# Performance work log

Hardware: AMD Instinct MI355X
Metric: run time of the kernel (lower is better)

## Reference

```python
import jax, jax.numpy as jnp
import numpy as np

H = 16            # num heads (sharded)
NOPE = 128        # qk_nope_head_dim
ROPE = 64         # qk_rope_head_dim
VD = 128          # v_head_dim
KV_RANK = 512
HEAD = NOPE + ROPE  # 192
SCALE = HEAD ** (-0.5)  # mscale == 1 (no yarn scaling)
EPS = 1e-6


def rmsnorm(x, w):
    var = jnp.mean(x * x, axis=-1, keepdims=True)
    return x * jax.lax.rsqrt(var + EPS) * w


def apply_rope(pe, cos, sin):
    # pe: [T, h, ROPE]; torch code de-interleaves pairs then applies
    # non-interleaved (rotate-half) rope: out = [e*cos - o*sin, o*cos + e*sin]
    e = pe[..., 0::2]
    o = pe[..., 1::2]
    c = cos[:, None, :]
    s = sin[:, None, :]
    return jnp.concatenate([e * c - o * s, o * c + e * s], axis=-1)


def setup_inputs() -> dict:
    key = jax.random.key(0)
    ks = jax.random.split(key, 10)
    T, D = 4096, 2048
    w = 0.02
    return {
        "hidden_states": jax.random.normal(ks[0], (T, D), jnp.float32),
        "cos": jax.random.uniform(ks[1], (T, ROPE // 2), jnp.float32),
        "sin": jax.random.uniform(ks[2], (T, ROPE // 2), jnp.float32),
        "w_q_a": jax.random.normal(ks[3], (D, 1536), jnp.float32) * w,
        "q_a_ln_w": jnp.ones((1536,), jnp.float32),
        "w_q_b": jax.random.normal(ks[4], (1536, H * HEAD), jnp.float32) * w,
        "w_kv_a": jax.random.normal(ks[5], (D, KV_RANK + ROPE), jnp.float32) * w,
        "kv_a_ln_w": jnp.ones((KV_RANK,), jnp.float32),
        "w_kv_b": jax.random.normal(ks[6], (KV_RANK, H * (NOPE + VD)), jnp.float32) * w,
        "w_o": jax.random.normal(ks[7], (H * VD, D), jnp.float32) * w,
        "batch_size": 2,
    }


def reference(hidden_states, cos, sin, w_q_a, q_a_ln_w, w_q_b, w_kv_a,
              kv_a_ln_w, w_kv_b, w_o, batch_size):
    T, D = hidden_states.shape
    B = int(batch_size)
    S = T // B

    # Q: low-rank down proj -> RMSNorm -> up proj
    q = rmsnorm(hidden_states @ w_q_a, q_a_ln_w) @ w_q_b
    q = q.reshape(T, H, HEAD)
    q_nope = q[..., :NOPE]
    q_pe = apply_rope(q[..., NOPE:], cos, sin)

    # KV: joint down proj with shared rope part (MQA-style)
    ckv = hidden_states @ w_kv_a                        # [T, 512+64]
    compressed_kv = ckv[:, :KV_RANK]
    k_pe = apply_rope(ckv[:, KV_RANK:][:, None, :], cos, sin)  # [T, 1, 64]
    kv = (rmsnorm(compressed_kv, kv_a_ln_w) @ w_kv_b).reshape(T, H, NOPE + VD)
    k_nope = kv[..., :NOPE]
    v = kv[..., NOPE:]                                   # [T, H, 128]

    # Assemble full query/key heads (value pad to 192 + final slice is a no-op
    # mathematically since padded dims are zero; we keep value dim = 128).
    query = jnp.concatenate([q_nope, q_pe], axis=-1)     # [T, H, 192]
    key = jnp.concatenate([k_nope, jnp.broadcast_to(k_pe, (T, H, ROPE))], axis=-1)

    # Causal (prefill) attention per sequence
    qb = query.reshape(B, S, H, HEAD)
    kb = key.reshape(B, S, H, HEAD)
    vb = v.reshape(B, S, H, VD)
    scores = jnp.einsum("bqhd,bkhd->bhqk", qb, kb) * SCALE
    causal = jnp.tril(jnp.ones((S, S), bool))
    scores = jnp.where(causal, scores, jnp.finfo(scores.dtype).min)
    probs = jax.nn.softmax(scores, axis=-1)
    attn = jnp.einsum("bhqk,bkhd->bqhd", probs, vb)      # [B, S, H, 128]

    return attn.reshape(T, H * VD) @ w_o
```

## Files before the change

kernel.cpp:

```cpp
#include <hip/hip_runtime.h>
#include <cstdint>
#include <cstddef>

#define TT 4096
#define DD 2048
#define NH 16
#define HEADD 192
#define NOPE 128
#define VDIM 128
#define SEQ 2048

typedef __bf16 bf16x8 __attribute__((ext_vector_type(8)));
typedef float f32x4 __attribute__((ext_vector_type(4)));
typedef unsigned int u32;

__device__ __forceinline__ float bf2f(unsigned short u) {
    union { unsigned int i; float f; } v; v.i = ((unsigned int)u) << 16; return v.f;
}
__device__ __forceinline__ unsigned short f2bf(float f) {
    union { float f; unsigned int i; } v; v.f = f;
    unsigned int r = v.i + 0x7FFFu + ((v.i >> 16) & 1u);
    return (unsigned short)(r >> 16);
}
__device__ __forceinline__ u32 pack2bf(float a, float b) {
    return (u32)f2bf(a) | ((u32)f2bf(b) << 16);
}
__device__ __forceinline__ void gload16(const unsigned short* g, unsigned short* l) {
    __builtin_amdgcn_global_load_lds((const __attribute__((address_space(1))) u32*)g,
                                     (__attribute__((address_space(3))) u32*)l, 16, 0, 0);
}

__global__ __launch_bounds__(256) void cvt_bf16_k(const float* __restrict__ x,
                                                  unsigned short* __restrict__ y, int n) {
    int i = (blockIdx.x * 256 + threadIdx.x) * 4;
    if (i < n) {
        float4 v = *(const float4*)(x + i);
        uint2 o;
        o.x = pack2bf(v.x, v.y);
        o.y = pack2bf(v.z, v.w);
        *(uint2*)(y + i) = o;
    }
}

__global__ __launch_bounds__(256) void transpose_cvt_k(const float* __restrict__ W,
                                                       unsigned short* __restrict__ Wt,
                                                       int K, int N) {
    __shared__ float tile[32][33];
    int n0 = blockIdx.x * 32, k0 = blockIdx.y * 32;
    int t = threadIdx.x, lr = t >> 5, lc = t & 31;
#pragma unroll
    for (int p = 0; p < 4; p++) {
        int k = k0 + lr + p * 8, n = n0 + lc;
        tile[lr + p * 8][lc] = (k < K && n < N) ? W[(size_t)k * N + n] : 0.f;
    }
    __syncthreads();
#pragma unroll
    for (int p = 0; p < 4; p++) {
        int n = n0 + lr + p * 8, k = k0 + lc;
        if (n < N && k < K) Wt[(size_t)n * K + k] = f2bf(tile[lc][lr + p * 8]);
    }
}

__global__ __launch_bounds__(256) void gemm_bf16_k(const unsigned short* __restrict__ A,
                                                   const unsigned short* __restrict__ Bt,
                                                   float* __restrict__ C,
                                                   int M, int N, int K) {
    __shared__ __align__(16) unsigned short As[128 * 32];
    __shared__ __align__(16) unsigned short Bs[128 * 32];
    int bm = blockIdx.y * 128, bn = blockIdx.x * 128;
    int t = threadIdx.x;
    int wave = t >> 6, lane = t & 63;
    int wr = (wave >> 1) * 64, wc = (wave & 1) * 64;
    int l15 = lane & 15, quad = lane >> 4;
    f32x4 acc[4][4];
    f32x4 zero = {0.f, 0.f, 0.f, 0.f};
#pragma unroll
    for (int i = 0; i < 4; i++)
#pragma unroll
        for (int j = 0; j < 4; j++) acc[i][j] = zero;
    int r0 = 16 * (2 * wave) + (lane >> 2);
    int cOff = (lane & 3) * 8;
    const unsigned short* gA0 = A + (size_t)(bm + r0) * K + cOff;
    const unsigned short* gA1 = A + (size_t)(bm + r0 + 16) * K + cOff;
    const unsigned short* gB0 = Bt + (size_t)(bn + r0) * K + cOff;
    const unsigned short* gB1 = Bt + (size_t)(bn + r0 + 16) * K + cOff;
    unsigned short* lA0 = &As[(2 * wave) * 512];
    unsigned short* lA1 = &As[(2 * wave + 1) * 512];
    unsigned short* lB0 = &Bs[(2 * wave) * 512];
    unsigned short* lB1 = &Bs[(2 * wave + 1) * 512];
    for (int k0 = 0; k0 < K; k0 += 32) {
        gload16(gA0 + k0, lA0);
        gload16(gA1 + k0, lA1);
        gload16(gB0 + k0, lB0);
        gload16(gB1 + k0, lB1);
        __syncthreads();
        bf16x8 af[4], bfr[4];
#pragma unroll
        for (int i = 0; i < 4; i++)
            af[i] = *(const bf16x8*)&As[(wr + i * 16 + l15) * 32 + quad * 8];
#pragma unroll
        for (int j = 0; j < 4; j++)
            bfr[j] = *(const bf16x8*)&Bs[(wc + j * 16 + l15) * 32 + quad * 8];
#pragma unroll
        for (int i = 0; i < 4; i++)
#pragma unroll
            for (int j = 0; j < 4; j++)
                acc[i][j] = __builtin_amdgcn_mfma_f32_16x16x32_bf16(af[i], bfr[j], acc[i][j], 0, 0, 0);
        __syncthreads();
    }
#pragma unroll
    for (int i = 0; i < 4; i++) {
        int row = bm + wr + i * 16 + quad * 4;
#pragma unroll
        for (int j = 0; j < 4; j++) {
            int col = bn + wc + j * 16 + l15;
            if (col < N) {
                float* cp = C + (size_t)row * N + col;
#pragma unroll
                for (int r = 0; r < 4; r++) cp[(size_t)r * N] = acc[i][j][r];
            }
        }
    }
}

__global__ __launch_bounds__(256) void gemm_bf16o_k(const unsigned short* __restrict__ A,
                                                    const unsigned short* __restrict__ Bt,
                                                    unsigned short* __restrict__ C,
                                                    int M, int N, int K) {
    __shared__ __align__(16) unsigned short As[128 * 32];
    __shared__ __align__(16) unsigned short Bs[128 * 32];
    int bm = blockIdx.y * 128, bn = blockIdx.x * 128;
    int t = threadIdx.x;
    int wave = t >> 6, lane = t & 63;
    int wr = (wave >> 1) * 64, wc = (wave & 1) * 64;
    int l15 = lane & 15, quad = lane >> 4;
    f32x4 acc[4][4];
    f32x4 zero = {0.f, 0.f, 0.f, 0.f};
#pragma unroll
    for (int i = 0; i < 4; i++)
#pragma unroll
        for (int j = 0; j < 4; j++) acc[i][j] = zero;
    int r0 = 16 * (2 * wave) + (lane >> 2);
    int cOff = (lane & 3) * 8;
    const unsigned short* gA0 = A + (size_t)(bm + r0) * K + cOff;
    const unsigned short* gA1 = A + (size_t)(bm + r0 + 16) * K + cOff;
    const unsigned short* gB0 = Bt + (size_t)(bn + r0) * K + cOff;
    const unsigned short* gB1 = Bt + (size_t)(bn + r0 + 16) * K + cOff;
    unsigned short* lA0 = &As[(2 * wave) * 512];
    unsigned short* lA1 = &As[(2 * wave + 1) * 512];
    unsigned short* lB0 = &Bs[(2 * wave) * 512];
    unsigned short* lB1 = &Bs[(2 * wave + 1) * 512];
    for (int k0 = 0; k0 < K; k0 += 32) {
        gload16(gA0 + k0, lA0);
        gload16(gA1 + k0, lA1);
        gload16(gB0 + k0, lB0);
        gload16(gB1 + k0, lB1);
        __syncthreads();
        bf16x8 af[4], bfr[4];
#pragma unroll
        for (int i = 0; i < 4; i++)
            af[i] = *(const bf16x8*)&As[(wr + i * 16 + l15) * 32 + quad * 8];
#pragma unroll
        for (int j = 0; j < 4; j++)
            bfr[j] = *(const bf16x8*)&Bs[(wc + j * 16 + l15) * 32 + quad * 8];
#pragma unroll
        for (int i = 0; i < 4; i++)
#pragma unroll
            for (int j = 0; j < 4; j++)
                acc[i][j] = __builtin_amdgcn_mfma_f32_16x16x32_bf16(af[i], bfr[j], acc[i][j], 0, 0, 0);
        __syncthreads();
    }
#pragma unroll
    for (int i = 0; i < 4; i++) {
        int row = bm + wr + i * 16 + quad * 4;
#pragma unroll
        for (int j = 0; j < 4; j++) {
            int col = bn + wc + j * 16 + l15;
            if (col < N) {
                unsigned short* cp = C + (size_t)row * N + col;
#pragma unroll
                for (int r = 0; r < 4; r++) cp[(size_t)r * N] = f2bf(acc[i][j][r]);
            }
        }
    }
}

#define KS_STRIDE 200
#define VT_STRIDE 72

__global__ __launch_bounds__(256) void gemm_kv_k(const unsigned short* __restrict__ A,
                                                 const unsigned short* __restrict__ Bt,
                                                 unsigned short* __restrict__ Kb2,
                                                 unsigned short* __restrict__ Vt2) {
    const int K = 512;
    __shared__ __align__(16) unsigned short As[128 * 32];
    __shared__ __align__(16) unsigned short Bs[128 * 32];
    int bm = blockIdx.y * 128, bn = blockIdx.x * 128;
    int t = threadIdx.x;
    int wave = t >> 6, lane = t & 63;
    int wr = (wave >> 1) * 64, wc = (wave & 1) * 64;
    int l15 = lane & 15, quad = lane >> 4;
    f32x4 acc[4][4];
    f32x4 zero = {0.f, 0.f, 0.f, 0.f};
#pragma unroll
    for (int i = 0; i < 4; i++)
#pragma unroll
        for (int j = 0; j < 4; j++) acc[i][j] = zero;
    int r0 = 16 * (2 * wave) + (lane >> 2);
    int cOff = (lane & 3) * 8;
    const unsigned short* gA0 = A + (size_t)(bm + r0) * K + cOff;
    const unsigned short* gA1 = A + (size_t)(bm + r0 + 16) * K + cOff;
    const unsigned short* gB0 = Bt + (size_t)(bn + r0) * K + cOff;
    const unsigned short* gB1 = Bt + (size_t)(bn + r0 + 16) * K + cOff;
    unsigned short* lA0 = &As[(2 * wave) * 512];
    unsigned short* lA1 = &As[(2 * wave + 1) * 512];
    unsigned short* lB0 = &Bs[(2 * wave) * 512];
    unsigned short* lB1 = &Bs[(2 * wave + 1) * 512];
    for (int k0 = 0; k0 < K; k0 += 32) {
        gload16(gA0 + k0, lA0);
        gload16(gA1 + k0, lA1);
        gload16(gB0 + k0, lB0);
        gload16(gB1 + k0, lB1);
        __syncthreads();
        bf16x8 af[4], bfr[4];
#pragma unroll
        for (int i = 0; i < 4; i++)
            af[i] = *(const bf16x8*)&As[(wr + i * 16 + l15) * 32 + quad * 8];
#pragma unroll
        for (int j = 0; j < 4; j++)
            bfr[j] = *(const bf16x8*)&Bs[(wc + j * 16 + l15) * 32 + quad * 8];
#pragma unroll
        for (int i = 0; i < 4; i++)
#pragma unroll
            for (int j = 0; j < 4; j++)
                acc[i][j] = __builtin_amdgcn_mfma_f32_16x16x32_bf16(af[i], bfr[j], acc[i][j], 0, 0, 0);
        __syncthreads();
    }
#pragma unroll
    for (int j = 0; j < 4; j++) {
        int col = bn + wc + j * 16 + l15;
        int h = col >> 8, dd = col & 255;
#pragma unroll
        for (int i = 0; i < 4; i++) {
            int row0 = bm + wr + i * 16 + quad * 4;
#pragma unroll
            for (int r = 0; r < 4; r++) {
                int row = row0 + r;
                int b = row >> 11, s = row & 2047;
                int kt = s >> 6, sr = s & 63;
                size_t bh = (size_t)(b * NH + h);
                unsigned short v = f2bf(acc[i][j][r]);
                if (dd < 128)
                    Kb2[((bh * 32 + kt) * 64 + sr) * KS_STRIDE + dd] = v;
                else
                    Vt2[((bh * 32 + kt) * 128 + (dd - 128)) * VT_STRIDE + sr] = v;
            }
        }
    }
}

__global__ __launch_bounds__(256) void kpe_fill_k(const unsigned short* __restrict__ kpe,
                                                  unsigned short* __restrict__ Kb2) {
    int trow = blockIdx.x, t = threadIdx.x;
    int b = trow >> 11, s = trow & 2047;
    int kt = s >> 6, sr = s & 63;
    const unsigned short* src = kpe + trow * 64;
#pragma unroll
    for (int i = t; i < NH * 64; i += 256) {
        int h = i >> 6, d = i & 63;
        Kb2[(((size_t)(b * NH + h) * 32 + kt) * 64 + sr) * KS_STRIDE + 128 + d] = src[d];
    }
}

__global__ __launch_bounds__(256) void rmsnorm_bf_k(const unsigned short* __restrict__ x,
                                                    const float* __restrict__ w,
                                                    unsigned short* __restrict__ y) {
    int row = blockIdx.x, t = threadIdx.x;
    const unsigned short* xr = x + (size_t)row * 2112;
    float s = 0.f;
    for (int i = t; i < 1536; i += 256) { float v = bf2f(xr[i]); s += v * v; }
    __shared__ float red[256];
    red[t] = s; __syncthreads();
    for (int o = 128; o > 0; o >>= 1) { if (t < o) red[t] += red[t + o]; __syncthreads(); }
    float scale = rsqrtf(red[0] / 1536.f + 1e-6f);
    unsigned short* yr = y + (size_t)row * 1536;
    for (int i = t; i < 1536; i += 256) yr[i] = f2bf(bf2f(xr[i]) * scale * w[i]);
}

__global__ __launch_bounds__(256) void kvprep_bf_k(const unsigned short* __restrict__ qab,
                                                   const float* __restrict__ w,
                                                   const float* __restrict__ cosb,
                                                   const float* __restrict__ sinb,
                                                   unsigned short* __restrict__ ckvn,
                                                   unsigned short* __restrict__ kpe) {
    int row = blockIdx.x, t = threadIdx.x;
    const unsigned short* xr = qab + (size_t)row * 2112 + 1536;
    float s = 0.f;
#pragma unroll
    for (int i = t; i < 512; i += 256) { float v = bf2f(xr[i]); s += v * v; }
    __shared__ float red[256];
    red[t] = s; __syncthreads();
    for (int o = 128; o > 0; o >>= 1) { if (t < o) red[t] += red[t + o]; __syncthreads(); }
    float scale = rsqrtf(red[0] / 512.f + 1e-6f);
    unsigned short* yr = ckvn + (size_t)row * 512;
#pragma unroll
    for (int i = t; i < 512; i += 256) yr[i] = f2bf(bf2f(xr[i]) * scale * w[i]);
    if (t < 32) {
        float e = bf2f(xr[512 + 2 * t]), o = bf2f(xr[512 + 2 * t + 1]);
        float c = cosb[row * 32 + t], sn = sinb[row * 32 + t];
        kpe[row * 64 + t]      = f2bf(e * c - o * sn);
        kpe[row * 64 + 32 + t] = f2bf(o * c + e * sn);
    }
}

__global__ __launch_bounds__(256) void qprep_bf_k(const unsigned short* __restrict__ q,
                                                  const float* __restrict__ cosb,
                                                  const float* __restrict__ sinb,
                                                  unsigned short* __restrict__ Qb) {
    const float SCALE = 0.07216878364870323f;
    int trow = blockIdx.x, t = threadIdx.x;
    const unsigned short* qr = q + (size_t)trow * (NH * HEADD);
    unsigned short* yr = Qb + (size_t)trow * (NH * HEADD);
    for (int i = t; i < NH * HEADD; i += 256) {
        int h = i / HEADD, d = i - h * HEADD;
        float val;
        if (d < NOPE) val = bf2f(qr[i]);
        else {
            int j = d - NOPE;
            int jj = j & 31;
            const unsigned short* pe = qr + h * HEADD + NOPE;
            float e = bf2f(pe[2 * jj]), o = bf2f(pe[2 * jj + 1]);
            float c = cosb[trow * 32 + jj], sn = sinb[trow * 32 + jj];
            val = (j < 32) ? (e * c - o * sn) : (o * c + e * sn);
        }
        yr[i] = f2bf(val * SCALE);
    }
}

__global__ __launch_bounds__(512) void attn_mfma_k(const unsigned short* __restrict__ Qb,
                                                   const unsigned short* __restrict__ Kb2,
                                                   const unsigned short* __restrict__ Vt2,
                                                   unsigned short* __restrict__ Opart,
                                                   float* __restrict__ Mbuf,
                                                   float* __restrict__ Lbuf) {
    __shared__ __align__(16) unsigned short Ks[64 * KS_STRIDE];
    __shared__ __align__(16) unsigned short Vts[128 * VT_STRIDE];
    int xe = 39 - blockIdx.x;
    int h  = blockIdx.y;
    int b  = blockIdx.z;
    int qt = 0, accn = 0;
    while (true) { int c = (qt >> 2) + 1; if (xe < accn + c) break; accn += c; qt++; }
    int chunk = xe - accn;
    int t = threadIdx.x;
    int w = t >> 6, lane = t & 63;
    int l15 = lane & 15, quad = lane >> 4;
    int bh = b * NH + h;
    int q0 = b * SEQ + qt * 128;
    int qglob = qt * 128 + w * 16 + l15;
    int flat = bh * 40 + xe;

    bf16x8 qf[6];
    {
        const unsigned short* qbase = Qb + ((size_t)(q0 + w * 16 + l15) * NH + h) * HEADD + quad * 8;
#pragma unroll
        for (int c = 0; c < 6; c++)
            qf[c] = *(const bf16x8*)(qbase + c * 32);
    }
    f32x4 acc_o[8];
    f32x4 zero = {0.f, 0.f, 0.f, 0.f};
#pragma unroll
    for (int j = 0; j < 8; j++) acc_o[j] = zero;
    float mrun = -1e30f, lrun = 0.f;

    int kt0 = chunk * 8, kt1 = min(kt0 + 7, 2 * qt + 1);
    int cbeg = w * 5 + min(w, 3), cnt = (w < 3) ? 6 : 5;
    for (int kt = kt0; kt <= kt1; kt++) {
        __syncthreads();
        {
            const unsigned short* kg = Kb2 + ((size_t)bh * 32 + kt) * (64 * KS_STRIDE) + lane * 8;
            const unsigned short* vg = Vt2 + ((size_t)bh * 32 + kt) * (128 * VT_STRIDE) + lane * 8;
            for (int c = cbeg; c < cbeg + cnt; c++) {
                if (c < 25) gload16(kg + c * 512, &Ks[c * 512]);
                else        gload16(vg + (c - 25) * 512, &Vts[(c - 25) * 512]);
            }
        }
        __syncthreads();
        f32x4 acc_s[4];
#pragma unroll
        for (int j = 0; j < 4; j++) acc_s[j] = zero;
#pragma unroll
        for (int c = 0; c < 6; c++) {
#pragma unroll
            for (int j = 0; j < 4; j++) {
                bf16x8 kf = *(const bf16x8*)&Ks[(j * 16 + l15) * KS_STRIDE + c * 32 + quad * 8];
                acc_s[j] = __builtin_amdgcn_mfma_f32_16x16x32_bf16(kf, qf[c], acc_s[j], 0, 0, 0);
            }
        }
        float sv[4][4];
#pragma unroll
        for (int j = 0; j < 4; j++) {
            int kbase = kt * 64 + j * 16 + quad * 4;
#pragma unroll
            for (int r = 0; r < 4; r++)
                sv[j][r] = (kbase + r > qglob) ? -1e30f : acc_s[j][r];
        }
        float v = sv[0][0];
#pragma unroll
        for (int j = 0; j < 4; j++)
#pragma unroll
            for (int r = 0; r < 4; r++) v = fmaxf(v, sv[j][r]);
        v = fmaxf(v, __shfl_xor(v, 16));
        v = fmaxf(v, __shfl_xor(v, 32));
        float mnew = fmaxf(mrun, v);
        float alpha = __expf(mrun - mnew);
        mrun = mnew;
        float rs = 0.f;
#pragma unroll
        for (int j = 0; j < 4; j++)
#pragma unroll
            for (int r = 0; r < 4; r++) { float p = __expf(sv[j][r] - mnew); sv[j][r] = p; rs += p; }
        rs += __shfl_xor(rs, 16);
        rs += __shfl_xor(rs, 32);
        lrun = lrun * alpha + rs;
        u32 pk[4][2];
#pragma unroll
        for (int j = 0; j < 4; j++) {
            pk[j][0] = pack2bf(sv[j][0], sv[j][1]);
            pk[j][1] = pack2bf(sv[j][2], sv[j][3]);
        }
#pragma unroll
        for (int jt = 0; jt < 8; jt++)
#pragma unroll
            for (int r = 0; r < 4; r++) acc_o[jt][r] *= alpha;
        int laneA = (((2 * quad) & 3) << 4) + l15;
        int laneB = (((2 * quad + 1) & 3) << 4) + l15;
        bool hi = (quad & 2) != 0;
#pragma unroll
        for (int c2 = 0; c2 < 2; c2++) {
            u32 a0 = __shfl(pk[2 * c2][0], laneA),     a1 = __shfl(pk[2 * c2][1], laneA);
            u32 b0 = __shfl(pk[2 * c2 + 1][0], laneA), b1 = __shfl(pk[2 * c2 + 1][1], laneA);
            u32 a2 = __shfl(pk[2 * c2][0], laneB),     a3 = __shfl(pk[2 * c2][1], laneB);
            u32 b2 = __shfl(pk[2 * c2 + 1][0], laneB), b3 = __shfl(pk[2 * c2 + 1][1], laneB);
            union { u32 d[4]; bf16x8 v8; } pf;
            pf.d[0] = hi ? b0 : a0;
            pf.d[1] = hi ? b1 : a1;
            pf.d[2] = hi ? b2 : a2;
            pf.d[3] = hi ? b3 : a3;
#pragma unroll
            for (int jt = 0; jt < 8; jt++) {
                bf16x8 vf = *(const bf16x8*)&Vts[(jt * 16 + l15) * VT_STRIDE + c2 * 32 + quad * 8];
                acc_o[jt] = __builtin_amdgcn_mfma_f32_16x16x32_bf16(vf, pf.v8, acc_o[jt], 0, 0, 0);
            }
        }
    }
    {
        int row = w * 16 + l15;
        unsigned short* op = Opart + (size_t)flat * 16384 + row * 128;
#pragma unroll
        for (int jt = 0; jt < 8; jt++)
#pragma unroll
            for (int r = 0; r < 4; r++)
                op[jt * 16 + quad * 4 + r] = f2bf(acc_o[jt][r]);
        if (quad == 0) {
            Mbuf[(size_t)flat * 128 + row] = mrun;
            Lbuf[(size_t)flat * 128 + row] = lrun;
        }
    }
}

__global__ __launch_bounds__(256) void attn_combine_k(const unsigned short* __restrict__ Opart,
                                                      const float* __restrict__ Mbuf,
                                                      const float* __restrict__ Lbuf,
                                                      unsigned short* __restrict__ attnb) {
    int q64 = blockIdx.x, h = blockIdx.y, b = blockIdx.z;
    int qt = q64 >> 1, half = q64 & 1;
    int nch = (qt >> 2) + 1;
    int F = 0;
    for (int q = 0; q < qt; q++) F += (q >> 2) + 1;
    int flat0 = (b * NH + h) * 40 + F;
    int t = threadIdx.x;
    int row = t >> 2, d0 = (t & 3) * 32;
    int row128 = half * 64 + row;
    float mc[4], lc[4], wgt[4];
    float mstar = -1e30f;
#pragma unroll
    for (int c = 0; c < 4; c++) {
        if (c < nch) {
            mc[c] = Mbuf[(size_t)(flat0 + c) * 128 + row128];
            lc[c] = Lbuf[(size_t)(flat0 + c) * 128 + row128];
        } else { mc[c] = -1e30f; lc[c] = 0.f; }
        mstar = fmaxf(mstar, mc[c]);
    }
    float L = 0.f;
#pragma unroll
    for (int c = 0; c < 4; c++) { wgt[c] = __expf(mc[c] - mstar); L += wgt[c] * lc[c]; }
    float invL = 1.f / L;
    float acc[32];
#pragma unroll
    for (int j = 0; j < 32; j++) acc[j] = 0.f;
#pragma unroll
    for (int c = 0; c < 4; c++) {
        if (c < nch) {
            const unsigned short* src = Opart + (size_t)(flat0 + c) * 16384 + row128 * 128 + d0;
            float wc = wgt[c];
#pragma unroll
            for (int g = 0; g < 4; g++) {
                uint4 u = *(const uint4*)(src + g * 8);
                const unsigned short* sp = (const unsigned short*)&u;
#pragma unroll
                for (int j = 0; j < 8; j++) acc[g * 8 + j] += wc * bf2f(sp[j]);
            }
        }
    }
    unsigned short* dst = attnb + (size_t)(b * SEQ + q64 * 64 + row) * 2048 + h * 128 + d0;
#pragma unroll
    for (int g = 0; g < 4; g++) {
        uint4 o;
        unsigned short* sp = (unsigned short*)&o;
#pragma unroll
        for (int j = 0; j < 8; j++) sp[j] = f2bf(acc[g * 8 + j] * invL);
        *(uint4*)(dst + g * 8) = o;
    }
}

extern "C" void kernel_launch(void* const* d_in, const int* in_sizes, int n_in,
                              void* d_out, int out_size, void* d_ws, size_t ws_size,
                              hipStream_t stream) {
    const float* hs     = (const float*)d_in[0];
    const float* cosb   = (const float*)d_in[1];
    const float* sinb   = (const float*)d_in[2];
    const float* w_q_a  = (const float*)d_in[3];
    const float* q_ln   = (const float*)d_in[4];
    const float* w_q_b  = (const float*)d_in[5];
    const float* w_kv_a = (const float*)d_in[6];
    const float* kv_ln  = (const float*)d_in[7];
    const float* w_kv_b = (const float*)d_in[8];
    const float* w_o    = (const float*)d_in[9];
    float* out = (float*)d_out;

    char* base = (char*)d_ws;
    size_t off = 0;
    auto take = [&](size_t bytes) { void* p = base + off; off += (bytes + 255) & ~(size_t)255; return p; };
    unsigned short* wqabT = (unsigned short*)take((size_t)2112 * 2048 * 2);
    unsigned short* wqbT  = (unsigned short*)take((size_t)3072 * 1536 * 2);
    unsigned short* wkvbT = (unsigned short*)take((size_t)4096 * 512 * 2);
    unsigned short* woT   = (unsigned short*)take((size_t)2048 * 2048 * 2);
    unsigned short* hsb   = (unsigned short*)take((size_t)TT * DD * 2);
    unsigned short* qab   = (unsigned short*)take((size_t)TT * 2112 * 2);
    unsigned short* qan   = (unsigned short*)take((size_t)TT * 1536 * 2);
    unsigned short* ckvn  = (unsigned short*)take((size_t)TT * 512 * 2);
    unsigned short* kpe   = (unsigned short*)take((size_t)TT * 64 * 2);
    unsigned short* qb3   = (unsigned short*)take((size_t)TT * 3072 * 2);
    unsigned short* Qbuf  = (unsigned short*)take((size_t)TT * NH * HEADD * 2);
    unsigned short* Kb2   = (unsigned short*)take((size_t)32 * 32 * 64 * KS_STRIDE * 2);
    unsigned short* Vt2   = (unsigned short*)take((size_t)32 * 32 * 128 * VT_STRIDE * 2);
    unsigned short* attnb = (unsigned short*)take((size_t)TT * 2048 * 2);
    unsigned short* Opart = (unsigned short*)take((size_t)1280 * 16384 * 2);
    float* Mbuf = (float*)take((size_t)1280 * 128 * 4);
    float* Lbuf = (float*)take((size_t)1280 * 128 * 4);

    cvt_bf16_k<<<(TT * DD) / 1024, 256, 0, stream>>>(hs, hsb, TT * DD);
    transpose_cvt_k<<<dim3(1536 / 32, 2048 / 32), 256, 0, stream>>>(w_q_a, wqabT, 2048, 1536);
    transpose_cvt_k<<<dim3(18, 2048 / 32), 256, 0, stream>>>(w_kv_a, wqabT + (size_t)1536 * 2048, 2048, 576);
    transpose_cvt_k<<<dim3(3072 / 32, 1536 / 32), 256, 0, stream>>>(w_q_b, wqbT, 1536, 3072);
    transpose_cvt_k<<<dim3(4096 / 32, 512 / 32), 256, 0, stream>>>(w_kv_b, wkvbT, 512, 4096);
    transpose_cvt_k<<<dim3(2048 / 32, 2048 / 32), 256, 0, stream>>>(w_o, woT, 2048, 2048);

    gemm_bf16o_k<<<dim3(17, 32), 256, 0, stream>>>(hsb, wqabT, qab, 4096, 2112, 2048);
    rmsnorm_bf_k<<<4096, 256, 0, stream>>>(qab, q_ln, qan);
    kvprep_bf_k<<<4096, 256, 0, stream>>>(qab, kv_ln, cosb, sinb, ckvn, kpe);
    gemm_bf16o_k<<<dim3(24, 32), 256, 0, stream>>>(qan, wqbT, qb3, 4096, 3072, 1536);
    qprep_bf_k<<<4096, 256, 0, stream>>>(qb3, cosb, sinb, Qbuf);
    gemm_kv_k<<<dim3(32, 32), 256, 0, stream>>>(ckvn, wkvbT, Kb2, Vt2);
    kpe_fill_k<<<4096, 256, 0, stream>>>(kpe, Kb2);
    attn_mfma_k<<<dim3(40, 16, 2), 512, 0, stream>>>(Qbuf, Kb2, Vt2, Opart, Mbuf, Lbuf);
    attn_combine_k<<<dim3(32, 16, 2), 256, 0, stream>>>(Opart, Mbuf, Lbuf, attnb);
    gemm_bf16_k<<<dim3(16, 32), 256, 0, stream>>>(attnb, woT, out, 4096, 2048, 2048);
}
```

Before: 544.2 us.

## Stage KV GEMM epilogue through LDS and add lazy softmax rescaling

Measured after the change: 527.4 us. 1.03x faster.

```diff
diff --git a/kernel.cpp b/kernel.cpp
--- a/kernel.cpp
+++ b/kernel.cpp
@@ -187,14 +187,17 @@
 
 #define KS_STRIDE 200
 #define VT_STRIDE 72
+#define CS_STRIDE 132
 
 __global__ __launch_bounds__(256) void gemm_kv_k(const unsigned short* __restrict__ A,
                                                  const unsigned short* __restrict__ Bt,
                                                  unsigned short* __restrict__ Kb2,
                                                  unsigned short* __restrict__ Vt2) {
     const int K = 512;
-    __shared__ __align__(16) unsigned short As[128 * 32];
-    __shared__ __align__(16) unsigned short Bs[128 * 32];
+    __shared__ __align__(16) unsigned short smem[128 * CS_STRIDE];
+    unsigned short* As = smem;
+    unsigned short* Bs = smem + 128 * 32;
+    unsigned short* Cs = smem;
     int bm = blockIdx.y * 128, bn = blockIdx.x * 128;
     int t = threadIdx.x;
     int wave = t >> 6, lane = t & 63;
@@ -237,24 +240,43 @@
         __syncthreads();
     }
 #pragma unroll
-    for (int j = 0; j < 4; j++) {
-        int col = bn + wc + j * 16 + l15;
-        int h = col >> 8, dd = col & 255;
-#pragma unroll
-        for (int i = 0; i < 4; i++) {
-            int row0 = bm + wr + i * 16 + quad * 4;
-#pragma unroll
-            for (int r = 0; r < 4; r++) {
-                int row = row0 + r;
-                int b = row >> 11, s = row & 2047;
-                int kt = s >> 6, sr = s & 63;
-                size_t bh = (size_t)(b * NH + h);
-                unsigned short v = f2bf(acc[i][j][r]);
-                if (dd < 128)
-                    Kb2[((bh * 32 + kt) * 64 + sr) * KS_STRIDE + dd] = v;
-                else
-                    Vt2[((bh * 32 + kt) * 128 + (dd - 128)) * VT_STRIDE + sr] = v;
-            }
+    for (int i = 0; i < 4; i++) {
+        int lr = wr + i * 16 + quad * 4;
+#pragma unroll
+        for (int j = 0; j < 4; j++) {
+            int lc = wc + j * 16 + l15;
+#pragma unroll
+            for (int r = 0; r < 4; r++)
+                Cs[(lr + r) * CS_STRIDE + lc] = f2bf(acc[i][j][r]);
+        }
+    }
+    __syncthreads();
+    int hh = bn >> 8;
+    bool isV = (bn & 255) != 0;
+    if (!isV) {
+        int row = t >> 1, halfc = t & 1;
+        int gs = bm + row;
+        int b2 = gs >> 11, s2 = gs & 2047;
+        unsigned short* dp = Kb2 +
+            ((size_t)((b2 * NH + hh) * 32 + (s2 >> 6)) * 64 + (s2 & 63)) * KS_STRIDE + halfc * 64;
+        const unsigned short* sp = &Cs[row * CS_STRIDE + halfc * 64];
+#pragma unroll
+        for (int g = 0; g < 8; g++)
+            *(uint4*)(dp + g * 8) = *(const uint4*)(sp + g * 8);
+    } else {
+        int kth = t >> 7, dim = t & 127;
+        int gs0 = bm + kth * 64;
+        int b2 = gs0 >> 11, s20 = gs0 & 2047;
+        unsigned short* dp = Vt2 +
+            ((size_t)((b2 * NH + hh) * 32 + (s20 >> 6)) * 128 + dim) * VT_STRIDE;
+#pragma unroll
+        for (int g = 0; g < 8; g++) {
+            uint4 o;
+            unsigned short* op = (unsigned short*)&o;
+#pragma unroll
+            for (int q2 = 0; q2 < 8; q2++)
+                op[q2] = Cs[(kth * 64 + g * 8 + q2) * CS_STRIDE + dim];
+            *(uint4*)(dp + g * 8) = o;
         }
     }
 }
@@ -397,12 +419,20 @@
             }
         }
         float sv[4][4];
-#pragma unroll
-        for (int j = 0; j < 4; j++) {
-            int kbase = kt * 64 + j * 16 + quad * 4;
-#pragma unroll
-            for (int r = 0; r < 4; r++)
-                sv[j][r] = (kbase + r > qglob) ? -1e30f : acc_s[j][r];
+        const bool needmask = (kt * 64 + 63) > (qt * 128 + w * 16);
+        if (needmask) {
+#pragma unroll
+            for (int j = 0; j < 4; j++) {
+                int kbase = kt * 64 + j * 16 + quad * 4;
+#pragma unroll
+                for (int r = 0; r < 4; r++)
+                    sv[j][r] = (kbase + r > qglob) ? -1e30f : acc_s[j][r];
+            }
+        } else {
+#pragma unroll
+            for (int j = 0; j < 4; j++)
+#pragma unroll
+                for (int r = 0; r < 4; r++) sv[j][r] = acc_s[j][r];
         }
         float v = sv[0][0];
 #pragma unroll
@@ -411,27 +441,30 @@
             for (int r = 0; r < 4; r++) v = fmaxf(v, sv[j][r]);
         v = fmaxf(v, __shfl_xor(v, 16));
         v = fmaxf(v, __shfl_xor(v, 32));
-        float mnew = fmaxf(mrun, v);
-        float alpha = __expf(mrun - mnew);
-        mrun = mnew;
+        if (!__all(v - mrun <= 8.f)) {
+            float mnew = fmaxf(mrun, v);
+            float alpha = __expf(mrun - mnew);
+            mrun = mnew;
+            lrun *= alpha;
+#pragma unroll
+            for (int jt = 0; jt < 8; jt++)
+#pragma unroll
+                for (int r = 0; r < 4; r++) acc_o[jt][r] *= alpha;
+        }
         float rs = 0.f;
 #pragma unroll
         for (int j = 0; j < 4; j++)
 #pragma unroll
-            for (int r = 0; r < 4; r++) { float p = __expf(sv[j][r] - mnew); sv[j][r] = p; rs += p; }
+            for (int r = 0; r < 4; r++) { float p = __expf(sv[j][r] - mrun); sv[j][r] = p; rs += p; }
         rs += __shfl_xor(rs, 16);
         rs += __shfl_xor(rs, 32);
-        lrun = lrun * alpha + rs;
+        lrun += rs;
         u32 pk[4][2];
 #pragma unroll
         for (int j = 0; j < 4; j++) {
             pk[j][0] = pack2bf(sv[j][0], sv[j][1]);
             pk[j][1] = pack2bf(sv[j][2], sv[j][3]);
         }
-#pragma unroll
-        for (int jt = 0; jt < 8; jt++)
-#pragma unroll
-            for (int r = 0; r < 4; r++) acc_o[jt][r] *= alpha;
         int laneA = (((2 * quad) & 3) << 4) + l15;
         int laneB = (((2 * quad + 1) & 3) << 4) + l15;
         bool hi = (quad & 2) != 0;
@@ -457,10 +490,12 @@
         int row = w * 16 + l15;
         unsigned short* op = Opart + (size_t)flat * 16384 + row * 128;
 #pragma unroll
-        for (int jt = 0; jt < 8; jt++)
-#pragma unroll
-            for (int r = 0; r < 4; r++)
-                op[jt * 16 + quad * 4 + r] = f2bf(acc_o[jt][r]);
+        for (int jt = 0; jt < 8; jt++) {
+            uint2 o;
+            o.x = pack2bf(acc_o[jt][0], acc_o[jt][1]);
+            o.y = pack2bf(acc_o[jt][2], acc_o[jt][3]);
+            *(uint2*)(op + jt * 16 + quad * 4) = o;
+        }
         if (quad == 0) {
             Mbuf[(size_t)flat * 128 + row] = mrun;
             Lbuf[(size_t)flat * 128 + row] = lrun;
```
